# Kernel tuning notes

Measured on AMD Instinct MI355X. Metric: run time of the kernel, lower is better.

## Reference

```python
import jax, jax.numpy as jnp
import numpy as np

N = 100000   # nodes
E = 1600000  # edges (before self loops)
IN = 128
H = 64
OUT = 10
G = 256      # graphs in batch
BN_EPS = 1e-5
NEG_SLOPE = 0.2


def setup_inputs() -> dict:
    key = jax.random.key(0)
    ks = jax.random.split(key, 24)
    def p(k, shape, fan_in):
        # glorot-ish init for weights
        s = 1.0 / np.sqrt(fan_in)
        return jax.random.uniform(k, shape, jnp.float32, -s, s)
    inp = {
        "x": jax.random.normal(ks[0], (N, IN), jnp.float32),
        "edge_index": jax.random.randint(ks[1], (2, E), 0, N),
        "batch": jnp.sort(jax.random.randint(ks[2], (N,), 0, G)),
        # GATConv 1 (in -> hidden, heads=1)
        "W1": p(ks[3], (IN, H), IN), "as1": p(ks[4], (H,), H), "ad1": p(ks[5], (H,), H), "b1": jnp.zeros((H,), jnp.float32),
        # GATConv 2 (hidden -> hidden)
        "W2": p(ks[6], (H, H), H), "as2": p(ks[7], (H,), H), "ad2": p(ks[8], (H,), H), "b2": jnp.zeros((H,), jnp.float32),
        # shared BatchNorm1d(hidden) params (bn1 reused twice)
        "bn_g": jnp.ones((H,), jnp.float32), "bn_b": jnp.zeros((H,), jnp.float32),
        # MLP head: hidden->64->16->8->out
        "m1_w": p(ks[9], (H, 64), H), "m1_b": jnp.zeros((64,), jnp.float32),
        "m2_w": p(ks[10], (64, 16), 64), "m2_b": jnp.zeros((16,), jnp.float32),
        "m3_w": p(ks[11], (16, 8), 16), "m3_b": jnp.zeros((8,), jnp.float32),
        "m4_w": p(ks[12], (8, OUT), 8), "m4_b": jnp.zeros((OUT,), jnp.float32),
    }
    return inp


def gat_conv(x, src, dst, W, a_src, a_dst, b, n):
    # PyG GATConv, heads=1, concat=True, negative_slope=0.2
    h = x @ W                                  # [n, H]
    alpha_s = h @ a_src                        # [n]
    alpha_d = h @ a_dst                        # [n]
    e = jax.nn.leaky_relu(alpha_s[src] + alpha_d[dst], NEG_SLOPE)  # [E']
    # segment softmax over incoming edges of each dst node
    emax = jax.ops.segment_max(e, dst, num_segments=n)
    w = jnp.exp(e - emax[dst])
    denom = jax.ops.segment_sum(w, dst, num_segments=n)
    alpha = w / denom[dst]
    out = jax.ops.segment_sum(h[src] * alpha[:, None], dst, num_segments=n)
    return out + b


def batch_norm(x, g, b):
    # training-mode BN over nodes
    m = jnp.mean(x, axis=0)
    v = jnp.mean((x - m) ** 2, axis=0)
    return (x - m) * jax.lax.rsqrt(v + BN_EPS) * g + b


def reference(x, edge_index, batch, W1, as1, ad1, b1, W2, as2, ad2, b2,
              bn_g, bn_b, m1_w, m1_b, m2_w, m2_b, m3_w, m3_b, m4_w, m4_b):
    n = x.shape[0]
    loop = jnp.arange(n, dtype=edge_index.dtype)
    src = jnp.concatenate([edge_index[0], loop])   # add self loops (PyG default)
    dst = jnp.concatenate([edge_index[1], loop])

    h = jax.nn.relu(gat_conv(x, src, dst, W1, as1, ad1, b1, n))
    h = batch_norm(h, bn_g, bn_b)
    h = jax.nn.relu(gat_conv(h, src, dst, W2, as2, ad2, b2, n))
    h = batch_norm(h, bn_g, bn_b)

    # global mean pool per graph
    s = jax.ops.segment_sum(h, batch, num_segments=G)                       # [G, H]
    cnt = jax.ops.segment_sum(jnp.ones((n,), h.dtype), batch, num_segments=G)
    pooled = s / jnp.maximum(cnt, 1.0)[:, None]

    z = jax.nn.relu(pooled @ m1_w + m1_b)
    z = jax.nn.relu(z @ m2_w + m2_b)
    z = jax.nn.relu(z @ m3_w + m3_b)
    return z @ m4_w + m4_b                                                  # [G, OUT]
```

## Files before the change

kernel.cpp:

```cpp
#include <hip/hip_runtime.h>
#include <hip/hip_fp16.h>

#define NN   100000
#define NE   1600000
#define ET   (NE + NN)
#define INF_ 128
#define HID  64
#define NG   256
#define BN_EPS 1e-5f
#define NEG  0.2f

#define BSPAN_LOG 8
#define BSPAN     (1 << BSPAN_LOG)
#define NBUK      ((NN + BSPAN - 1) / BSPAN)
#define BUKCAP    5120
#define P1_EPT    16
#define P1_CHUNK  (256 * P1_EPT)

__device__ __forceinline__ float lrelu(float v) { return v > 0.f ? v : NEG * v; }

__device__ __forceinline__ float readlane_f(float v, int l) {
  return __int_as_float(__builtin_amdgcn_readlane(__float_as_int(v), l));
}

__global__ __launch_bounds__(256) void init_k(
    int* __restrict__ bukcur,
    float* __restrict__ fsum1, float* __restrict__ fsq1,
    float* __restrict__ fsum2, float* __restrict__ fsq2,
    float* __restrict__ pooled, float* __restrict__ cnt) {
  int i = blockIdx.x * 256 + threadIdx.x;
  if (i < NBUK) bukcur[i] = i * BUKCAP;
  if (i < HID) { fsum1[i] = 0.f; fsq1[i] = 0.f; fsum2[i] = 0.f; fsq2[i] = 0.f; }
  if (i < NG * HID) pooled[i] = 0.f;
  if (i < NG) cnt[i] = 0.f;
}

__global__ __launch_bounds__(256) void part1_k(const int* __restrict__ ei,
                                               int* __restrict__ bukcur,
                                               int2* __restrict__ stage) {
  __shared__ int hist[NBUK];
  __shared__ int base[NBUK];
  int t = threadIdx.x;
  for (int b = t; b < NBUK; b += 256) hist[b] = 0;
  __syncthreads();
  int chunk = blockIdx.x * P1_CHUNK;
  int myb[P1_EPT], myr[P1_EPT], mys[P1_EPT], myd[P1_EPT];
#pragma unroll
  for (int it = 0; it < P1_EPT; ++it) {
    int i = chunk + it * 256 + t;
    bool v = i < ET;
    int src = 0, dst = 0;
    if (v) {
      src = i < NE ? ei[i] : i - NE;
      dst = i < NE ? ei[NE + i] : i - NE;
    }
    myb[it] = v ? (dst >> BSPAN_LOG) : -1;
    mys[it] = src;
    myd[it] = dst;
    myr[it] = v ? atomicAdd(&hist[dst >> BSPAN_LOG], 1) : 0;
  }
  __syncthreads();
  for (int b = t; b < NBUK; b += 256)
    base[b] = hist[b] ? atomicAdd(&bukcur[b], hist[b]) : 0;
  __syncthreads();
#pragma unroll
  for (int it = 0; it < P1_EPT; ++it)
    if (myb[it] >= 0)
      stage[base[myb[it]] + myr[it]] = make_int2(mys[it], myd[it]);
}

__global__ __launch_bounds__(512) void bukscan_k(const int* __restrict__ bukcur,
                                                 int* __restrict__ bukbase,
                                                 int* __restrict__ rowptr) {
  __shared__ int sh[512];
  int t = threadIdx.x;
  int c = (t < NBUK) ? (bukcur[t] - t * BUKCAP) : 0;
  sh[t] = c;
  __syncthreads();
  for (int off = 1; off < 512; off <<= 1) {
    int add = (t >= off) ? sh[t - off] : 0;
    __syncthreads();
    sh[t] += add;
    __syncthreads();
  }
  if (t < NBUK) bukbase[t] = sh[t] - c;
  if (t == 0) rowptr[NN] = ET;
}

__global__ __launch_bounds__(256) void part2_k(const int2* __restrict__ stage,
                                               const int* __restrict__ bukcur,
                                               const int* __restrict__ bukbase,
                                               int* __restrict__ rowptr,
                                               int* __restrict__ esrc) {
  __shared__ int lcnt[BSPAN];
  __shared__ int lscan[BSPAN];
  int b = blockIdx.x;
  int node0 = b << BSPAN_LOG;
  int t = threadIdx.x;
  lcnt[t] = 0;
  __syncthreads();
  int s = b * BUKCAP, e = bukcur[b];
  for (int i = s + t; i < e; i += 256)
    atomicAdd(&lcnt[stage[i].y - node0], 1);
  __syncthreads();
  int v = lcnt[t];
  lscan[t] = v;
  __syncthreads();
  for (int off = 1; off < 256; off <<= 1) {
    int add = (t >= off) ? lscan[t - off] : 0;
    __syncthreads();
    lscan[t] += add;
    __syncthreads();
  }
  int excl = bukbase[b] + lscan[t] - v;
  if (node0 + t < NN) rowptr[node0 + t] = excl;
  lcnt[t] = excl;
  __syncthreads();
  for (int i = s + t; i < e; i += 256) {
    int2 p = stage[i];
    int pos = atomicAdd(&lcnt[p.y - node0], 1);
    esrc[pos] = p.x;
  }
}

template <int K, bool STATS>
__global__ __launch_bounds__(256) void gemm_att(
    const float* __restrict__ x,
    const float* __restrict__ fsum, const float* __restrict__ fsq,
    const float* __restrict__ bng, const float* __restrict__ bnb,
    const float* __restrict__ W,
    const float* __restrict__ a_s, const float* __restrict__ a_d,
    __half* __restrict__ h, float* __restrict__ sv_out, float* __restrict__ dv_out) {
  __shared__ float Wl[K * HID];
  __shared__ float cvec[HID];
  __shared__ float scl[HID], shf[HID];
  int tid = threadIdx.x;
  if (tid < HID) {
    cvec[tid] = 0.f;
    if (STATS) {
      float m = fsum[tid] * (1.0f / NN);
      float v = fsq[tid] * (1.0f / NN) - m * m;
      float a = bng[tid] * rsqrtf(v + BN_EPS);
      scl[tid] = a;
      shf[tid] = bnb[tid] - m * a;
    }
  }
  __syncthreads();
  if (STATS) {
    float clocal = 0.f;
    for (int i = tid; i < K * HID; i += 256) {
      int k = i >> 6;
      float w = W[i];
      clocal += shf[k] * w;
      Wl[i] = w * scl[k];
    }
    atomicAdd(&cvec[tid & 63], clocal);
  } else {
    for (int i = tid; i < K * HID; i += 256) Wl[i] = W[i];
  }
  __syncthreads();

  int lane = tid & 63;
  int wid = tid >> 6;
  int row0 = blockIdx.x * 16 + wid * 4;
  int ur = __builtin_amdgcn_readfirstlane(row0);
  const float* xr0 = x + (size_t)ur * K;
  const float* xr1 = xr0 + K;
  const float* xr2 = xr0 + 2 * K;
  const float* xr3 = xr0 + 3 * K;
  float cv = cvec[lane];
  float a0 = cv, a1 = cv, a2 = cv, a3 = cv;
#pragma unroll 4
  for (int k = 0; k < K; k += 4) {
    float4 v0 = *(const float4*)(xr0 + k);
    float4 v1 = *(const float4*)(xr1 + k);
    float4 v2 = *(const float4*)(xr2 + k);
    float4 v3 = *(const float4*)(xr3 + k);
    float w0 = Wl[(k + 0) * HID + lane];
    float w1 = Wl[(k + 1) * HID + lane];
    float w2 = Wl[(k + 2) * HID + lane];
    float w3 = Wl[(k + 3) * HID + lane];
    a0 = fmaf(v0.x, w0, a0); a0 = fmaf(v0.y, w1, a0);
    a0 = fmaf(v0.z, w2, a0); a0 = fmaf(v0.w, w3, a0);
    a1 = fmaf(v1.x, w0, a1); a1 = fmaf(v1.y, w1, a1);
    a1 = fmaf(v1.z, w2, a1); a1 = fmaf(v1.w, w3, a1);
    a2 = fmaf(v2.x, w0, a2); a2 = fmaf(v2.y, w1, a2);
    a2 = fmaf(v2.z, w2, a2); a2 = fmaf(v2.w, w3, a2);
    a3 = fmaf(v3.x, w0, a3); a3 = fmaf(v3.y, w1, a3);
    a3 = fmaf(v3.z, w2, a3); a3 = fmaf(v3.w, w3, a3);
  }

  float asl = a_s[lane], adl = a_d[lane];
  h[(size_t)(row0 + 0) * HID + lane] = __float2half(a0);
  h[(size_t)(row0 + 1) * HID + lane] = __float2half(a1);
  h[(size_t)(row0 + 2) * HID + lane] = __float2half(a2);
  h[(size_t)(row0 + 3) * HID + lane] = __float2half(a3);
  float s0 = a0 * asl, d0 = a0 * adl;
  float s1 = a1 * asl, d1 = a1 * adl;
  float s2 = a2 * asl, d2 = a2 * adl;
  float s3 = a3 * asl, d3 = a3 * adl;
  for (int o = 32; o; o >>= 1) {
    s0 += __shfl_xor(s0, o); d0 += __shfl_xor(d0, o);
    s1 += __shfl_xor(s1, o); d1 += __shfl_xor(d1, o);
    s2 += __shfl_xor(s2, o); d2 += __shfl_xor(d2, o);
    s3 += __shfl_xor(s3, o); d3 += __shfl_xor(d3, o);
  }
  if (lane == 0) {
    sv_out[row0 + 0] = s0; dv_out[row0 + 0] = d0;
    sv_out[row0 + 1] = s1; dv_out[row0 + 1] = d1;
    sv_out[row0 + 2] = s2; dv_out[row0 + 2] = d2;
    sv_out[row0 + 3] = s3; dv_out[row0 + 3] = d3;
  }
}

__device__ __forceinline__ float2 gat_node_half(
    int node, int start, int deg, const int* __restrict__ esrc,
    const float* __restrict__ s, const float* __restrict__ d,
    const __half* __restrict__ h, int lane32, int base, int fl) {
  float dn = d[node];
  int j = start + (lane32 < deg ? lane32 : 0);
  int sj = esrc[j];
  float e = lrelu(s[sj] + dn);
  float ev = (lane32 < deg) ? e : -INFINITY;
  float m = ev;
  for (int o = 16; o; o >>= 1) m = fmaxf(m, __shfl_xor(m, o));
  float w = (lane32 < deg) ? __expf(e - m) : 0.f;
  float wsum = w;
  for (int o = 16; o; o >>= 1) wsum += __shfl_xor(wsum, o);
  float alpha = w / wsum;
  float2 acc = {0.f, 0.f};
  for (int t = 0; t < deg; t += 4) {
#pragma unroll
    for (int i = 0; i < 4; ++i) {
      int p = __shfl(sj, base + t + i);
      float a = __shfl(alpha, base + t + i);
      unsigned off = ((unsigned)p << 6) + fl;
      float2 hv = __half22float2(*(const __half2*)&h[off]);
      acc.x = fmaf(a, hv.x, acc.x);
      acc.y = fmaf(a, hv.y, acc.y);
    }
  }
  return acc;
}

__device__ float2 gat_node_full(
    int node, const int* __restrict__ rowptr, const int* __restrict__ esrc,
    const float* __restrict__ s, const float* __restrict__ d,
    const __half* __restrict__ h, int lane, int half, int fl) {
  int start = rowptr[node], end = rowptr[node + 1];
  int deg = end - start;
  float dn = d[node];
  float2 acc = {0.f, 0.f};
  if (deg <= 64) {
    int j = start + (lane < deg ? lane : 0);
    int sj = esrc[j];
    float e = lrelu(s[sj] + dn);
    float ev = (lane < deg) ? e : -INFINITY;
    float m = ev;
    for (int o = 32; o; o >>= 1) m = fmaxf(m, __shfl_xor(m, o));
    float w = (lane < deg) ? __expf(e - m) : 0.f;
    float wsum = w;
    for (int o = 32; o; o >>= 1) wsum += __shfl_xor(wsum, o);
    float alpha = w / wsum;
    for (int t = 0; t < deg; t += 8) {
#pragma unroll
      for (int i = 0; i < 4; ++i) {
        int e0 = t + 2 * i;
        int p0 = __builtin_amdgcn_readlane(sj, e0);
        int p1 = __builtin_amdgcn_readlane(sj, e0 + 1);
        float a0 = readlane_f(alpha, e0);
        float a1 = readlane_f(alpha, e0 + 1);
        int ps = half ? p1 : p0;
        float aw = half ? a1 : a0;
        unsigned off = ((unsigned)ps << 6) + fl;
        float2 hv = __half22float2(*(const __half2*)&h[off]);
        acc.x = fmaf(aw, hv.x, acc.x);
        acc.y = fmaf(aw, hv.y, acc.y);
      }
    }
  } else {
    float m = -INFINITY;
    for (int j = start + lane; j < end; j += 64)
      m = fmaxf(m, lrelu(s[esrc[j]] + dn));
    for (int o = 32; o; o >>= 1) m = fmaxf(m, __shfl_xor(m, o));
    float wsum = 0.f;
    for (int j = start + lane; j < end; j += 64)
      wsum += __expf(lrelu(s[esrc[j]] + dn) - m);
    for (int o = 32; o; o >>= 1) wsum += __shfl_xor(wsum, o);
    float inv = 1.0f / wsum;
    for (int cb = start; cb < end; cb += 64) {
      int cc = min(64, end - cb);
      int j = cb + (lane < cc ? lane : 0);
      int sj = esrc[j];
      float alpha = (lane < cc) ? __expf(lrelu(s[sj] + dn) - m) * inv : 0.f;
      for (int t = 0; t < cc; t += 8) {
#pragma unroll
        for (int i = 0; i < 4; ++i) {
          int e0 = t + 2 * i;
          int p0 = __builtin_amdgcn_readlane(sj, e0);
          int p1 = __builtin_amdgcn_readlane(sj, e0 + 1);
          float a0 = readlane_f(alpha, e0);
          float a1 = readlane_f(alpha, e0 + 1);
          int ps = half ? p1 : p0;
          float aw = half ? a1 : a0;
          unsigned off = ((unsigned)ps << 6) + fl;
          float2 hv = __half22float2(*(const __half2*)&h[off]);
          acc.x = fmaf(aw, hv.x, acc.x);
          acc.y = fmaf(aw, hv.y, acc.y);
        }
      }
    }
  }
  acc.x += __shfl_xor(acc.x, 32);
  acc.y += __shfl_xor(acc.y, 32);
  return acc;
}

__device__ __forceinline__ float2 gat_pair(
    int nA, const int* __restrict__ rowptr, const int* __restrict__ esrc,
    const float* __restrict__ s, const float* __restrict__ d,
    const __half* __restrict__ h, int lane, int half, int lane32, int fl) {
  int nB = nA + 1;
  int sA = rowptr[nA], sB = rowptr[nB], eB = rowptr[nB + 1];
  int degA = sB - sA, degB = eB - sB;
  if (degA <= 32 && degB <= 32) {
    int node = half ? nB : nA;
    int start = half ? sB : sA;
    int deg = half ? degB : degA;
    return gat_node_half(node, start, deg, esrc, s, d, h, lane32, half << 5, fl);
  }
  float2 aA = gat_node_full(nA, rowptr, esrc, s, d, h, lane, half, fl);
  float2 aB = gat_node_full(nB, rowptr, esrc, s, d, h, lane, half, fl);
  return half ? aB : aA;
}

__global__ __launch_bounds__(256) void gat_agg_k(
    const int* __restrict__ rowptr, const int* __restrict__ esrc,
    const float* __restrict__ s, const float* __restrict__ d,
    const __half* __restrict__ h, const float* __restrict__ bias,
    float* __restrict__ y, float* __restrict__ fsum, float* __restrict__ fsq) {
  __shared__ float lsum[HID], lsq[HID];
  int tid = threadIdx.x;
  if (tid < HID) { lsum[tid] = 0.f; lsq[tid] = 0.f; }
  __syncthreads();
  int lane = tid & 63;
  int half = lane >> 5;
  int lane32 = lane & 31;
  int fl = lane32 * 2;
  float2 bv = *(const float2*)&bias[fl];
  float2 ls = {0.f, 0.f}, lq = {0.f, 0.f};
  int wave = blockIdx.x * 4 + (tid >> 6);
  int nwaves = gridDim.x * 4;
  for (int p = wave; p < NN / 2; p += nwaves) {
    int nA = 2 * p;
    float2 acc = gat_pair(nA, rowptr, esrc, s, d, h, lane, half, lane32, fl);
    float vx = fmaxf(acc.x + bv.x, 0.f);
    float vy = fmaxf(acc.y + bv.y, 0.f);
    int node = nA + half;
    *(float2*)&y[(size_t)node * HID + fl] = make_float2(vx, vy);
    ls.x += vx; ls.y += vy;
    lq.x += vx * vx; lq.y += vy * vy;
  }
  atomicAdd(&lsum[fl + 0], ls.x);
  atomicAdd(&lsum[fl + 1], ls.y);
  atomicAdd(&lsq[fl + 0], lq.x);
  atomicAdd(&lsq[fl + 1], lq.y);
  __syncthreads();
  if (tid < HID) { atomicAdd(&fsum[tid], lsum[tid]); atomicAdd(&fsq[tid], lsq[tid]); }
}

__global__ __launch_bounds__(256) void gat_agg_pool_k(
    const int* __restrict__ rowptr, const int* __restrict__ esrc,
    const float* __restrict__ s, const float* __restrict__ d,
    const __half* __restrict__ h, const float* __restrict__ bias,
    const int* __restrict__ batch, float* __restrict__ pooled,
    float* __restrict__ cnt, float* __restrict__ fsum, float* __restrict__ fsq) {
  __shared__ float lsum[HID], lsq[HID];
  int tid = threadIdx.x;
  if (tid < HID) { lsum[tid] = 0.f; lsq[tid] = 0.f; }
  __syncthreads();
  int lane = tid & 63;
  int half = lane >> 5;
  int lane32 = lane & 31;
  int fl = lane32 * 2;
  float2 bv = *(const float2*)&bias[fl];
  float2 ls = {0.f, 0.f}, lq = {0.f, 0.f};
  int wave = blockIdx.x * 4 + (tid >> 6);
  int nwaves = gridDim.x * 4;
  int per = (((NN / 2) + nwaves - 1) / nwaves) * 2;
  int lo = wave * per, hi = min(lo + per, NN);
  if (lo < hi) {
    int g = batch[lo + half];
    float2 pacc = {0.f, 0.f};
    float c = 0.f;
    for (int nA = lo; nA < hi; nA += 2) {
      int myn = nA + half;
      int bg = batch[myn];
      if (bg != g) {
        atomicAdd(&pooled[g * HID + fl + 0], pacc.x);
        atomicAdd(&pooled[g * HID + fl + 1], pacc.y);
        if (lane32 == 0) atomicAdd(&cnt[g], c);
        g = bg; pacc.x = 0.f; pacc.y = 0.f; c = 0.f;
      }
      float2 acc = gat_pair(nA, rowptr, esrc, s, d, h, lane, half, lane32, fl);
      float vx = fmaxf(acc.x + bv.x, 0.f);
      float vy = fmaxf(acc.y + bv.y, 0.f);
      pacc.x += vx; pacc.y += vy; c += 1.f;
      ls.x += vx; ls.y += vy;
      lq.x += vx * vx; lq.y += vy * vy;
    }
    atomicAdd(&pooled[g * HID + fl + 0], pacc.x);
    atomicAdd(&pooled[g * HID + fl + 1], pacc.y);
    if (lane32 == 0) atomicAdd(&cnt[g], c);
  }
  atomicAdd(&lsum[fl + 0], ls.x);
  atomicAdd(&lsum[fl + 1], ls.y);
  atomicAdd(&lsq[fl + 0], lq.x);
  atomicAdd(&lsq[fl + 1], lq.y);
  __syncthreads();
  if (tid < HID) { atomicAdd(&fsum[tid], lsum[tid]); atomicAdd(&fsq[tid], lsq[tid]); }
}

__global__ __launch_bounds__(64) void mlp_head(
    const float* __restrict__ pooled, const float* __restrict__ cnt,
    const float* __restrict__ fsum, const float* __restrict__ fsq,
    const float* __restrict__ bng, const float* __restrict__ bnb,
    const float* __restrict__ m1w, const float* __restrict__ m1b,
    const float* __restrict__ m2w, const float* __restrict__ m2b,
    const float* __restrict__ m3w, const float* __restrict__ m3b,
    const float* __restrict__ m4w, const float* __restrict__ m4b,
    float* __restrict__ out) {
  __shared__ float p[64], z1[64], z2[16], z3[8];
  int g = blockIdx.x, f = threadIdx.x;
  float m = fsum[f] * (1.0f / NN);
  float v = fsq[f] * (1.0f / NN) - m * m;
  float a = bng[f] * rsqrtf(v + BN_EPS);
  float c = bnb[f] - m * a;
  float cv = fmaxf(cnt[g], 1.0f);
  p[f] = a * pooled[g * 64 + f] / cv + c;
  __syncthreads();
  float a1 = m1b[f];
  for (int k = 0; k < 64; ++k) a1 += p[k] * m1w[k * 64 + f];
  z1[f] = fmaxf(a1, 0.f);
  __syncthreads();
  if (f < 16) {
    float a2 = m2b[f];
    for (int k = 0; k < 64; ++k) a2 += z1[k] * m2w[k * 16 + f];
    z2[f] = fmaxf(a2, 0.f);
  }
  __syncthreads();
  if (f < 8) {
    float a3 = m3b[f];
    for (int k = 0; k < 16; ++k) a3 += z2[k] * m3w[k * 8 + f];
    z3[f] = fmaxf(a3, 0.f);
  }
  __syncthreads();
  if (f < 10) {
    float a4 = m4b[f];
    for (int k = 0; k < 8; ++k) a4 += z3[k] * m4w[k * 10 + f];
    out[g * 10 + f] = a4;
  }
}

extern "C" void kernel_launch(void* const* d_in, const int* in_sizes, int n_in,
                              void* d_out, int out_size, void* d_ws, size_t ws_size,
                              hipStream_t stream) {
  const float* x   = (const float*)d_in[0];
  const int*   ei  = (const int*)d_in[1];
  const int*   bat = (const int*)d_in[2];
  const float* W1  = (const float*)d_in[3];
  const float* as1 = (const float*)d_in[4];
  const float* ad1 = (const float*)d_in[5];
  const float* b1  = (const float*)d_in[6];
  const float* W2  = (const float*)d_in[7];
  const float* as2 = (const float*)d_in[8];
  const float* ad2 = (const float*)d_in[9];
  const float* b2  = (const float*)d_in[10];
  const float* bng = (const float*)d_in[11];
  const float* bnb = (const float*)d_in[12];
  const float* m1w = (const float*)d_in[13];
  const float* m1b = (const float*)d_in[14];
  const float* m2w = (const float*)d_in[15];
  const float* m2b = (const float*)d_in[16];
  const float* m3w = (const float*)d_in[17];
  const float* m3b = (const float*)d_in[18];
  const float* m4w = (const float*)d_in[19];
  const float* m4b = (const float*)d_in[20];
  float* out = (float*)d_out;

  float* ws = (float*)d_ws;
  size_t off = 0;
  __half* hbuf = (__half*)(ws + off); off += (size_t)NN * HID / 2;
  float* ybuf = ws + off; off += (size_t)NN * HID;
  float* sbuf = ws + off; off += NN;
  float* dbuf = ws + off; off += NN;
  int* rowptr = (int*)(ws + off); off += NN + 1;
  int* esrc   = (int*)(ws + off); off += ET;
  int* bukcur = (int*)(ws + off); off += NBUK;
  int* bukbase = (int*)(ws + off); off += NBUK;
  float* fsum1 = ws + off; off += HID;
  float* fsq1  = ws + off; off += HID;
  float* fsum2 = ws + off; off += HID;
  float* fsq2  = ws + off; off += HID;
  float* pooled = ws + off; off += (size_t)NG * HID;
  float* cnt  = ws + off; off += NG;
  int2* stage = (int2*)ybuf;

  dim3 b256(256);
  const int gemmGrid = NN / 16;
  const int p1Grid = (ET + P1_CHUNK - 1) / P1_CHUNK;
  const int aggGrid = 2048;

  init_k<<<(NG * HID + 255) / 256, b256, 0, stream>>>(bukcur, fsum1, fsq1,
                                                      fsum2, fsq2, pooled, cnt);
  part1_k<<<p1Grid, b256, 0, stream>>>(ei, bukcur, stage);
  bukscan_k<<<1, 512, 0, stream>>>(bukcur, bukbase, rowptr);
  part2_k<<<NBUK, b256, 0, stream>>>(stage, bukcur, bukbase, rowptr, esrc);

  gemm_att<INF_, false><<<gemmGrid, b256, 0, stream>>>(
      x, nullptr, nullptr, nullptr, nullptr, W1, as1, ad1, hbuf, sbuf, dbuf);
  gat_agg_k<<<aggGrid, b256, 0, stream>>>(rowptr, esrc, sbuf, dbuf, hbuf, b1,
                                          ybuf, fsum1, fsq1);

  gemm_att<HID, true><<<gemmGrid, b256, 0, stream>>>(
      ybuf, fsum1, fsq1, bng, bnb, W2, as2, ad2, hbuf, sbuf, dbuf);
  gat_agg_pool_k<<<aggGrid, b256, 0, stream>>>(rowptr, esrc, sbuf, dbuf, hbuf,
                                               b2, bat, pooled, cnt, fsum2, fsq2);

  mlp_head<<<NG, 64, 0, stream>>>(pooled, cnt, fsum2, fsq2, bng, bnb,
                                  m1w, m1b, m2w, m2b, m3w, m3b, m4w, m4b, out);
}
```

Before: 375.9 us.

## Merge edge partition pass with first GEMM and fold bucket scan into part2

The first edge-bucketing pass and the layer-1 feature GEMM now run as one launch, with blocks split by index between the two independent jobs and sharing dynamic LDS. The separate single-block bucket-scan kernel is removed: each part2 block computes its own bucket base by reducing the counts of the preceding buckets, and rowptr[NN] is written in init. This removes two launches and lets the GEMM overlap the partition. Each part2 block now does redundant prefix work, and the aggregation grid size changes from 2048 to 3125.

```diff
diff --git a/kernel.cpp b/kernel.cpp
--- a/kernel.cpp
+++ b/kernel.cpp
@@ -16,6 +16,8 @@
 #define BUKCAP    5120
 #define P1_EPT    16
 #define P1_CHUNK  (256 * P1_EPT)
+#define P1_GRID   ((ET + P1_CHUNK - 1) / P1_CHUNK)
+#define GEMM_GRID (NN / 16)
 
 __device__ __forceinline__ float lrelu(float v) { return v > 0.f ? v : NEG * v; }
 
@@ -24,26 +26,27 @@
 }
 
 __global__ __launch_bounds__(256) void init_k(
-    int* __restrict__ bukcur,
+    int* __restrict__ bukcur, int* __restrict__ rowptr,
     float* __restrict__ fsum1, float* __restrict__ fsq1,
     float* __restrict__ fsum2, float* __restrict__ fsq2,
     float* __restrict__ pooled, float* __restrict__ cnt) {
   int i = blockIdx.x * 256 + threadIdx.x;
+  if (i == 0) rowptr[NN] = ET;
   if (i < NBUK) bukcur[i] = i * BUKCAP;
   if (i < HID) { fsum1[i] = 0.f; fsq1[i] = 0.f; fsum2[i] = 0.f; fsq2[i] = 0.f; }
   if (i < NG * HID) pooled[i] = 0.f;
   if (i < NG) cnt[i] = 0.f;
 }
 
-__global__ __launch_bounds__(256) void part1_k(const int* __restrict__ ei,
-                                               int* __restrict__ bukcur,
-                                               int2* __restrict__ stage) {
-  __shared__ int hist[NBUK];
-  __shared__ int base[NBUK];
+__device__ __forceinline__ void part1_core(
+    float* smem, const int* __restrict__ ei, int* __restrict__ bukcur,
+    int2* __restrict__ stage, int blk) {
+  int* hist = (int*)smem;
+  int* base = hist + NBUK;
   int t = threadIdx.x;
   for (int b = t; b < NBUK; b += 256) hist[b] = 0;
   __syncthreads();
-  int chunk = blockIdx.x * P1_CHUNK;
+  int chunk = blk * P1_CHUNK;
   int myb[P1_EPT], myr[P1_EPT], mys[P1_EPT], myd[P1_EPT];
 #pragma unroll
   for (int it = 0; it < P1_EPT; ++it) {
@@ -69,71 +72,15 @@
       stage[base[myb[it]] + myr[it]] = make_int2(mys[it], myd[it]);
 }
 
-__global__ __launch_bounds__(512) void bukscan_k(const int* __restrict__ bukcur,
-                                                 int* __restrict__ bukbase,
-                                                 int* __restrict__ rowptr) {
-  __shared__ int sh[512];
-  int t = threadIdx.x;
-  int c = (t < NBUK) ? (bukcur[t] - t * BUKCAP) : 0;
-  sh[t] = c;
-  __syncthreads();
-  for (int off = 1; off < 512; off <<= 1) {
-    int add = (t >= off) ? sh[t - off] : 0;
-    __syncthreads();
-    sh[t] += add;
-    __syncthreads();
-  }
-  if (t < NBUK) bukbase[t] = sh[t] - c;
-  if (t == 0) rowptr[NN] = ET;
-}
-
-__global__ __launch_bounds__(256) void part2_k(const int2* __restrict__ stage,
-                                               const int* __restrict__ bukcur,
-                                               const int* __restrict__ bukbase,
-                                               int* __restrict__ rowptr,
-                                               int* __restrict__ esrc) {
-  __shared__ int lcnt[BSPAN];
-  __shared__ int lscan[BSPAN];
-  int b = blockIdx.x;
-  int node0 = b << BSPAN_LOG;
-  int t = threadIdx.x;
-  lcnt[t] = 0;
-  __syncthreads();
-  int s = b * BUKCAP, e = bukcur[b];
-  for (int i = s + t; i < e; i += 256)
-    atomicAdd(&lcnt[stage[i].y - node0], 1);
-  __syncthreads();
-  int v = lcnt[t];
-  lscan[t] = v;
-  __syncthreads();
-  for (int off = 1; off < 256; off <<= 1) {
-    int add = (t >= off) ? lscan[t - off] : 0;
-    __syncthreads();
-    lscan[t] += add;
-    __syncthreads();
-  }
-  int excl = bukbase[b] + lscan[t] - v;
-  if (node0 + t < NN) rowptr[node0 + t] = excl;
-  lcnt[t] = excl;
-  __syncthreads();
-  for (int i = s + t; i < e; i += 256) {
-    int2 p = stage[i];
-    int pos = atomicAdd(&lcnt[p.y - node0], 1);
-    esrc[pos] = p.x;
-  }
-}
-
 template <int K, bool STATS>
-__global__ __launch_bounds__(256) void gemm_att(
+__device__ __forceinline__ void gemm_core(
+    float* Wl, float* cvec, float* scl, float* shf, int blk,
     const float* __restrict__ x,
     const float* __restrict__ fsum, const float* __restrict__ fsq,
     const float* __restrict__ bng, const float* __restrict__ bnb,
     const float* __restrict__ W,
     const float* __restrict__ a_s, const float* __restrict__ a_d,
     __half* __restrict__ h, float* __restrict__ sv_out, float* __restrict__ dv_out) {
-  __shared__ float Wl[K * HID];
-  __shared__ float cvec[HID];
-  __shared__ float scl[HID], shf[HID];
   int tid = threadIdx.x;
   if (tid < HID) {
     cvec[tid] = 0.f;
@@ -162,7 +109,7 @@
 
   int lane = tid & 63;
   int wid = tid >> 6;
-  int row0 = blockIdx.x * 16 + wid * 4;
+  int row0 = blk * 16 + wid * 4;
   int ur = __builtin_amdgcn_readfirstlane(row0);
   const float* xr0 = x + (size_t)ur * K;
   const float* xr1 = xr0 + K;
@@ -210,6 +157,82 @@
     sv_out[row0 + 1] = s1; dv_out[row0 + 1] = d1;
     sv_out[row0 + 2] = s2; dv_out[row0 + 2] = d2;
     sv_out[row0 + 3] = s3; dv_out[row0 + 3] = d3;
+  }
+}
+
+__global__ __launch_bounds__(256) void p1_gemm1_k(
+    const int* __restrict__ ei, int* __restrict__ bukcur, int2* __restrict__ stage,
+    const float* __restrict__ x, const float* __restrict__ W1,
+    const float* __restrict__ as1, const float* __restrict__ ad1,
+    __half* __restrict__ h, float* __restrict__ sv, float* __restrict__ dv) {
+  extern __shared__ float smem[];
+  if (blockIdx.x < P1_GRID) {
+    part1_core(smem, ei, bukcur, stage, blockIdx.x);
+  } else {
+    float* Wl = smem;
+    float* cvec = Wl + INF_ * HID;
+    gemm_core<INF_, false>(Wl, cvec, nullptr, nullptr, (int)blockIdx.x - P1_GRID,
+                           x, nullptr, nullptr, nullptr, nullptr, W1, as1, ad1,
+                           h, sv, dv);
+  }
+}
+
+template <int K, bool STATS>
+__global__ __launch_bounds__(256) void gemm_att(
+    const float* __restrict__ x,
+    const float* __restrict__ fsum, const float* __restrict__ fsq,
+    const float* __restrict__ bng, const float* __restrict__ bnb,
+    const float* __restrict__ W,
+    const float* __restrict__ a_s, const float* __restrict__ a_d,
+    __half* __restrict__ h, float* __restrict__ sv_out, float* __restrict__ dv_out) {
+  __shared__ float Wl[K * HID];
+  __shared__ float cvec[HID];
+  __shared__ float scl[HID], shf[HID];
+  gemm_core<K, STATS>(Wl, cvec, scl, shf, blockIdx.x, x, fsum, fsq, bng, bnb,
+                      W, a_s, a_d, h, sv_out, dv_out);
+}
+
+__global__ __launch_bounds__(256) void part2_k(const int2* __restrict__ stage,
+                                               const int* __restrict__ bukcur,
+                                               int* __restrict__ rowptr,
+                                               int* __restrict__ esrc) {
+  __shared__ int lcnt[BSPAN];
+  __shared__ int lscan[BSPAN];
+  int b = blockIdx.x;
+  int node0 = b << BSPAN_LOG;
+  int t = threadIdx.x;
+  int partial = 0;
+  for (int i = t; i < b; i += 256) partial += bukcur[i] - i * BUKCAP;
+  lscan[t] = partial;
+  __syncthreads();
+  for (int off = 128; off; off >>= 1) {
+    if (t < off) lscan[t] += lscan[t + off];
+    __syncthreads();
+  }
+  int bbase = lscan[0];
+  lcnt[t] = 0;
+  __syncthreads();
+  int s = b * BUKCAP, e = bukcur[b];
+  for (int i = s + t; i < e; i += 256)
+    atomicAdd(&lcnt[stage[i].y - node0], 1);
+  __syncthreads();
+  int v = lcnt[t];
+  lscan[t] = v;
+  __syncthreads();
+  for (int off = 1; off < 256; off <<= 1) {
+    int add = (t >= off) ? lscan[t - off] : 0;
+    __syncthreads();
+    lscan[t] += add;
+    __syncthreads();
+  }
+  int excl = bbase + lscan[t] - v;
+  if (node0 + t < NN) rowptr[node0 + t] = excl;
+  lcnt[t] = excl;
+  __syncthreads();
+  for (int i = s + t; i < e; i += 256) {
+    int2 p = stage[i];
+    int pos = atomicAdd(&lcnt[p.y - node0], 1);
+    esrc[pos] = p.x;
   }
 }
 
@@ -497,7 +520,6 @@
   int* rowptr = (int*)(ws + off); off += NN + 1;
   int* esrc   = (int*)(ws + off); off += ET;
   int* bukcur = (int*)(ws + off); off += NBUK;
-  int* bukbase = (int*)(ws + off); off += NBUK;
   float* fsum1 = ws + off; off += HID;
   float* fsq1  = ws + off; off += HID;
   float* fsum2 = ws + off; off += HID;
@@ -507,22 +529,20 @@
   int2* stage = (int2*)ybuf;
 
   dim3 b256(256);
-  const int gemmGrid = NN / 16;
-  const int p1Grid = (ET + P1_CHUNK - 1) / P1_CHUNK;
-  const int aggGrid = 2048;
-
-  init_k<<<(NG * HID + 255) / 256, b256, 0, stream>>>(bukcur, fsum1, fsq1,
-                                                      fsum2, fsq2, pooled, cnt);
-  part1_k<<<p1Grid, b256, 0, stream>>>(ei, bukcur, stage);
-  bukscan_k<<<1, 512, 0, stream>>>(bukcur, bukbase, rowptr);
-  part2_k<<<NBUK, b256, 0, stream>>>(stage, bukcur, bukbase, rowptr, esrc);
-
-  gemm_att<INF_, false><<<gemmGrid, b256, 0, stream>>>(
-      x, nullptr, nullptr, nullptr, nullptr, W1, as1, ad1, hbuf, sbuf, dbuf);
+  const int aggGrid = 3125;
+  const size_t fusedLds = (size_t)(INF_ * HID + HID) * sizeof(float);
+
+  init_k<<<(NG * HID + 255) / 256, b256, 0, stream>>>(bukcur, rowptr, fsum1,
+                                                      fsq1, fsum2, fsq2,
+                                                      pooled, cnt);
+  p1_gemm1_k<<<P1_GRID + GEMM_GRID, b256, fusedLds, stream>>>(
+      ei, bukcur, stage, x, W1, as1, ad1, hbuf, sbuf, dbuf);
+  part2_k<<<NBUK, b256, 0, stream>>>(stage, bukcur, rowptr, esrc);
+
   gat_agg_k<<<aggGrid, b256, 0, stream>>>(rowptr, esrc, sbuf, dbuf, hbuf, b1,
                                           ybuf, fsum1, fsq1);
 
-  gemm_att<HID, true><<<gemmGrid, b256, 0, stream>>>(
+  gemm_att<HID, true><<<GEMM_GRID, b256, 0, stream>>>(
       ybuf, fsum1, fsq1, bng, bnb, W2, as2, ad2, hbuf, sbuf, dbuf);
   gat_agg_pool_k<<<aggGrid, b256, 0, stream>>>(rowptr, esrc, sbuf, dbuf, hbuf,
                                                b2, bat, pooled, cnt, fsum2, fsq2);
```

Result: slower. 419.7 us (+11.6%).
